# Kernel tuning notes

Measured on AMD Instinct MI355X. Metric: run time of the kernel, lower is better.

The kernel has to match this reference:

```python
import jax, jax.numpy as jnp
import numpy as np

B, T, D = 4, 2048, 2048
H = 16
DH = D // H  # 128
THETA = 10000.0


def _rope(x, offset=0):
    # x: [b, h, t, d]; lucidrains rotary_embedding_torch style (interleaved pairs)
    d = x.shape[-1]
    t = x.shape[-2]
    inv_freq = 1.0 / (THETA ** (jnp.arange(0, d, 2, dtype=jnp.float32) / d))  # [d/2]
    pos = jnp.arange(offset, offset + t, dtype=jnp.float32)
    freqs = pos[:, None] * inv_freq[None, :]              # [t, d/2]
    freqs = jnp.repeat(freqs, 2, axis=-1)                 # [t, d] (n r) interleave
    cos = jnp.cos(freqs).astype(x.dtype)
    sin = jnp.sin(freqs).astype(x.dtype)
    x1 = x[..., 0::2]
    x2 = x[..., 1::2]
    rot = jnp.stack([-x2, x1], axis=-1).reshape(x.shape)  # rotate_half
    return x * cos + rot * sin


def setup_inputs() -> dict:
    key = jax.random.key(0)
    ks = jax.random.split(key, 5)
    s = 1.0 / np.sqrt(D)
    return {
        "x": jax.random.normal(ks[0], (B, T, D), jnp.float32),
        "Wq": jax.random.normal(ks[1], (D, D), jnp.float32) * s,
        "Wk": jax.random.normal(ks[2], (D, D), jnp.float32) * s,
        "Wv": jax.random.normal(ks[3], (D, D), jnp.float32) * s,
        "Wo": jax.random.normal(ks[4], (D, D), jnp.float32) * s,
    }


def reference(x, Wq, Wk, Wv, Wo):
    b, t, d = x.shape
    # QKV projections (bias-free), split heads: b t (h f) -> b h t f
    q = (x @ Wq).reshape(b, t, H, DH).transpose(0, 2, 1, 3)
    k = (x @ Wk).reshape(b, t, H, DH).transpose(0, 2, 1, 3)
    v = (x @ Wv).reshape(b, t, H, DH).transpose(0, 2, 1, 3)
    # rotary embedding on q and k (offset = 0)
    q = _rope(q)
    k = _rope(k)
    # causal scaled dot-product attention
    scale = 1.0 / np.sqrt(DH)
    logits = jnp.einsum('bhtf,bhsf->bhts', q, k) * scale
    causal = jnp.tril(jnp.ones((t, t), dtype=bool))
    logits = jnp.where(causal, logits, jnp.finfo(logits.dtype).min)
    p = jax.nn.softmax(logits, axis=-1)
    y = jnp.einsum('bhts,bhsf->bhtf', p, v)
    # b h t f -> b t (h f), then output projection
    y = y.transpose(0, 2, 1, 3).reshape(b, t, d)
    return y @ Wo
```

## Files before the change

### kernel.cpp

```cpp
#include <hip/hip_runtime.h>
#include <hip/hip_bf16.h>
#include <math.h>

typedef unsigned short u16;
typedef __attribute__((ext_vector_type(8))) __bf16 bf16x8;
typedef __attribute__((ext_vector_type(4))) float f32x4;
typedef __attribute__((ext_vector_type(16))) float f32x16;
typedef __attribute__((ext_vector_type(8))) u16 u16x8;
typedef __attribute__((ext_vector_type(4))) u16 u16x4;
typedef __attribute__((ext_vector_type(4))) unsigned u32x4;

#define T_SEQ 2048
#define DMODEL 2048
#define NH 16
#define DHEAD 128
#define BATCH 4
#define QKV_STR 6144
#define ATTN_SCALE 0.08838834764831845f
#define QSCALE_LOG2E 0.1275411278534803f
#define ROPE_EXP_C  -0.20762050593045857f

#define GLOAD(gp, lp) __builtin_amdgcn_global_load_lds( \
    (const __attribute__((address_space(1))) void*)(gp), \
    (__attribute__((address_space(3))) void*)(lp), 16, 0, 0)

#define BAR() __builtin_amdgcn_s_barrier()
#define VMCNT4() asm volatile("s_waitcnt vmcnt(4)" ::: "memory")
#define MFMA32(A, B, C) __builtin_amdgcn_mfma_f32_32x32x16_bf16(A, B, C, 0, 0, 0)

__device__ __forceinline__ float b2f(u16 u) {
  union { float f; unsigned int i; } x; x.i = ((unsigned int)u) << 16; return x.f;
}
__device__ __forceinline__ u16 f2b(float f) {
  __bf16 h = (__bf16)f;
  return *(u16*)&h;
}
__device__ __forceinline__ unsigned pk2(float lo, float hi2) {
  __bf16 a = (__bf16)lo, b = (__bf16)hi2;
  unsigned short ua = *(unsigned short*)&a, ub = *(unsigned short*)&b;
  return (unsigned)ua | ((unsigned)ub << 16);
}

__global__ __launch_bounds__(256) void cast_f32_bf16(const float* __restrict__ in,
                                                     u16* __restrict__ out) {
  long i = ((long)blockIdx.x * 256 + threadIdx.x) * 8;
  float4 a = *(const float4*)(in + i);
  float4 b = *(const float4*)(in + i + 4);
  u16x8 r;
  r[0] = f2b(a.x); r[1] = f2b(a.y); r[2] = f2b(a.z); r[3] = f2b(a.w);
  r[4] = f2b(b.x); r[5] = f2b(b.y); r[6] = f2b(b.z); r[7] = f2b(b.w);
  *(u16x8*)(out + i) = r;
}

__global__ __launch_bounds__(256) void wtrans4_kernel(const float* __restrict__ W0,
                                                      const float* __restrict__ W1,
                                                      const float* __restrict__ W2,
                                                      const float* __restrict__ W3,
                                                      u16* __restrict__ WtBase) {
  __shared__ float tile[64][65];
  const int z = blockIdx.z;
  const float* W = (z == 0) ? W0 : (z == 1) ? W1 : (z == 2) ? W2 : W3;
  u16* Wt = WtBase + (long)z * 4194304;
  const int k0 = blockIdx.x * 64, n0 = blockIdx.y * 64;
  const int c = threadIdx.x & 63, r4 = threadIdx.x >> 6;
#pragma unroll
  for (int p = 0; p < 16; p++) {
    int r = p * 4 + r4;
    tile[r][c] = W[(long)(k0 + r) * DMODEL + n0 + c];
  }
  __syncthreads();
#pragma unroll
  for (int p = 0; p < 16; p++) {
    int r = p * 4 + r4;
    Wt[(long)(n0 + r) * DMODEL + k0 + c] = f2b(tile[c][r]);
  }
}

__global__ __launch_bounds__(256) void vtrans_kernel(const u16* __restrict__ C,
                                                     u16* __restrict__ Vt) {
  __shared__ u16 tile[64][66];
  const int s0 = blockIdx.x * 64, f0 = blockIdx.y * 64;
  const int bh = blockIdx.z;
  const int b = bh >> 4, h = bh & 15;
  const int c = threadIdx.x & 63, r4 = threadIdx.x >> 6;
#pragma unroll
  for (int p = 0; p < 16; p++) {
    int r = p * 4 + r4;
    tile[r][c] = C[(long)(b * T_SEQ + s0 + r) * QKV_STR + 4096 + h * DHEAD + f0 + c];
  }
  __syncthreads();
#pragma unroll
  for (int p = 0; p < 16; p++) {
    int r = p * 4 + r4;
    Vt[(long)(bh * DHEAD + f0 + r) * T_SEQ + s0 + c] = tile[c][r];
  }
}

__global__ __launch_bounds__(256) void rope_k_kernel(u16* __restrict__ X) {
  int idx = blockIdx.x * 256 + threadIdx.x;
  int c8 = idx & 255;
  long row = idx >> 8;
  int t = (int)(row & (T_SEQ - 1));
  int i4 = c8 & 15;
  long off = row * QKV_STR + 2048 + (long)c8 * 8;
  u16x8 v = *(u16x8*)(X + off);
  float o[8];
#pragma unroll
  for (int j = 0; j < 4; j++) {
    int i = i4 * 4 + j;
    float inv = __builtin_amdgcn_exp2f((float)i * ROPE_EXP_C);
    float ang = (float)t * inv;
    float cs = __cosf(ang), sn = __sinf(ang);
    float x0 = b2f(v[2 * j]), x1 = b2f(v[2 * j + 1]);
    o[2 * j]     = x0 * cs - x1 * sn;
    o[2 * j + 1] = x1 * cs + x0 * sn;
  }
  u16x8 r;
#pragma unroll
  for (int j = 0; j < 8; j++) r[j] = f2b(o[j]);
  *(u16x8*)(X + off) = r;
}

#define LOAD_A(q)                                                      \
  _Pragma("unroll") for (int k = 0; k < 2; k++)                        \
  _Pragma("unroll") for (int m = 0; m < 2; m++) {                      \
    int r = wr * 128 + (q) * 32 + m * 16 + lr;                         \
    int cc = (k * 4 + lc) ^ (r & 7);                                   \
    a[k][m] = *(const bf16x8*)&sA[par][r * 64 + cc * 8];               \
  }

#define LOAD_B()                                                       \
  _Pragma("unroll") for (int k = 0; k < 2; k++)                        \
  _Pragma("unroll") for (int n = 0; n < 4; n++) {                      \
    int r = wc * 64 + n * 16 + lr;                                     \
    int cc = (k * 4 + lc) ^ (r & 7);                                   \
    b[k][n] = *(const bf16x8*)&sB[par][r * 64 + cc * 8];               \
  }

#define MFMA_QUAD(q)                                                   \
  _Pragma("unroll") for (int k = 0; k < 2; k++)                        \
  _Pragma("unroll") for (int n = 0; n < 4; n++)                        \
  _Pragma("unroll") for (int m = 0; m < 2; m++)                        \
    acc[(q) * 2 + m][n] = __builtin_amdgcn_mfma_f32_16x16x32_bf16(     \
        a[k][m], b[k][n], acc[(q) * 2 + m][n], 0, 0, 0);

#define STAGE_HALF(g, ld, ldsp, rc0, t_, h_)                           \
  _Pragma("unroll") for (int j = 0; j < 2; j++) {                      \
    int rl = (h_) * 128 + wid * 16 + j * 8 + (lane >> 3);              \
    int cc = (lane & 7) ^ (lane >> 3);                                 \
    GLOAD((g) + ((rc0) + rl) * (long)(ld) + (long)(t_) * 64 + cc * 8,  \
          (ldsp) + (h_) * 128 * 64 + (wid * 16 + j * 8) * 64);         \
  }

template <int OUT_F32>
__global__ __launch_bounds__(512, 2) void gemm_bt(const u16* __restrict__ A, long lda,
                                                  const u16* __restrict__ Bt,
                                                  void* __restrict__ Cv,
                                                  int M, int N, int K) {
  __shared__ u16 sA[2][256 * 64];
  __shared__ u16 sB[2][256 * 64];
  const int tid = threadIdx.x, lane = tid & 63, wid = tid >> 6;
  const int wr = wid >> 2, wc = wid & 3;
  const int lr = lane & 15, lc = lane >> 4;
  const int id = blockIdx.x;
  const int per = (N >> 8) >> 3;
  const int g8 = id >> 3;
  const long col0 = (long)((id & 7) + 8 * (g8 % per)) * 256;
  const long row0 = (long)(g8 / per) * 256;
  const int NT = K >> 6;

  f32x4 acc[8][4] = {};
  bf16x8 a[2][2], b[2][4];

  STAGE_HALF(Bt, K, &sB[0][0], col0, 0, 0);
  STAGE_HALF(Bt, K, &sB[0][0], col0, 0, 1);
  STAGE_HALF(A, lda, &sA[0][0], row0, 0, 0);
  STAGE_HALF(A, lda, &sA[0][0], row0, 0, 1);
  STAGE_HALF(Bt, K, &sB[1][0], col0, 1, 0);
  STAGE_HALF(Bt, K, &sB[1][0], col0, 1, 1);
  VMCNT4();
  BAR();

#pragma unroll 2
  for (int t = 0; t < NT; t++) {
    const int par = t & 1;
    LOAD_B();
    LOAD_A(0);
    if (t + 1 < NT) { STAGE_HALF(A, lda, &sA[par ^ 1][0], row0, t + 1, 0); }
    BAR();
    __builtin_amdgcn_s_setprio(1); MFMA_QUAD(0); __builtin_amdgcn_s_setprio(0);
    BAR();
    LOAD_A(1);
    if (t + 1 < NT) { STAGE_HALF(A, lda, &sA[par ^ 1][0], row0, t + 1, 1); }
    if (t + 2 < NT) { STAGE_HALF(Bt, K, &sB[par][0], col0, t + 2, 0); }
    BAR();
    __builtin_amdgcn_s_setprio(1); MFMA_QUAD(1); __builtin_amdgcn_s_setprio(0);
    BAR();
    LOAD_A(2);
    if (t + 2 < NT) { STAGE_HALF(Bt, K, &sB[par][0], col0, t + 2, 1); }
    BAR();
    __builtin_amdgcn_s_setprio(1); MFMA_QUAD(2); __builtin_amdgcn_s_setprio(0);
    BAR();
    LOAD_A(3);
    VMCNT4();
    BAR();
    __builtin_amdgcn_s_setprio(1); MFMA_QUAD(3); __builtin_amdgcn_s_setprio(0);
    BAR();
  }

#pragma unroll
  for (int mf = 0; mf < 8; mf++)
#pragma unroll
    for (int n = 0; n < 4; n++)
#pragma unroll
      for (int i = 0; i < 4; i++) {
        long row = row0 + wr * 128 + mf * 16 + lc * 4 + i;
        long col = col0 + wc * 64 + n * 16 + lr;
        float v = acc[mf][n][i];
        if (OUT_F32) ((float*)Cv)[row * N + col] = v;
        else ((u16*)Cv)[row * N + col] = f2b(v);
      }
}

__global__ __launch_bounds__(256, 2) void attn_kernel(const u16* __restrict__ QK,
                                                      const u16* __restrict__ Vt) {
  __shared__ u16 lK[2][64 * 128];
  __shared__ u16 lV[2][128 * 64];
  const int tid = threadIdx.x, lane = tid & 63, w = tid >> 6;
  const int hi = lane >> 5, l31 = lane & 31;
  const int id = blockIdx.x;
  const int qt = 15 - (id >> 6);
  const int bh = id & 63;
  const int b = bh >> 4, h = bh & 15;
  const int qg = qt * 128 + w * 32 + l31;
  const int swz = l31 & 7;

  bf16x8 qf[8];
  const long qrow = (long)(b * T_SEQ + qg) * QKV_STR + h * DHEAD;
#pragma unroll
  for (int kd = 0; kd < 8; kd++) {
    u16x8 raw = *(const u16x8*)(QK + qrow + kd * 16 + hi * 8);
    bf16x8 q;
#pragma unroll
    for (int jj = 0; jj < 4; jj++) {
      int pi = kd * 8 + hi * 4 + jj;
      float ang = (float)qg * __builtin_amdgcn_exp2f((float)pi * ROPE_EXP_C);
      float cs = __cosf(ang), sn = __sinf(ang);
      float x0 = b2f(raw[2 * jj]), x1 = b2f(raw[2 * jj + 1]);
      q[2 * jj]     = (__bf16)((x0 * cs - x1 * sn) * QSCALE_LOG2E);
      q[2 * jj + 1] = (__bf16)((x1 * cs + x0 * sn) * QSCALE_LOG2E);
    }
    qf[kd] = q;
  }

  f32x16 o0 = {}, o1 = {}, o2 = {}, o3 = {};
  float m_st = -INFINITY, l_st = 0.f;
  const int nt = (qt + 1) * 2;

#define STAGE(nb, kt_)                                                              \
  {                                                                                 \
    _Pragma("unroll")                                                               \
    for (int j = 0; j < 4; j++) {                                                   \
      int sb = (w * 4 + j) * 64;                                                    \
      int slot = sb + lane;                                                         \
      { int r = slot >> 4, pc = slot & 15, cc = pc ^ (r & 7);                       \
        GLOAD(QK + (long)(b * T_SEQ + (kt_) * 64 + r) * QKV_STR + 2048 +            \
                  h * DHEAD + cc * 8,                                               \
              &lK[nb][sb * 8]); }                                                   \
      { int r = slot >> 3, pc = slot & 7, cc = pc ^ (r & 7);                        \
        GLOAD(Vt + (long)(bh * DHEAD + r) * T_SEQ + (kt_) * 64 + cc * 8,            \
              &lV[nb][sb * 8]); }                                                   \
    }                                                                               \
  }

  STAGE(0, 0);
  __syncthreads();

  for (int kt = 0; kt < nt; kt++) {
    const int cur = kt & 1;
    if (kt + 1 < nt) STAGE(cur ^ 1, kt + 1);

    f32x16 st0 = {}, st1 = {};
    __builtin_amdgcn_s_setprio(1);
#pragma unroll
    for (int kd = 0; kd < 8; kd++) {
      int pc = (kd * 2 + hi) ^ swz;
      bf16x8 kf0 = *(const bf16x8*)&lK[cur][l31 * 128 + pc * 8];
      bf16x8 kf1 = *(const bf16x8*)&lK[cur][(32 + l31) * 128 + pc * 8];
      st0 = MFMA32(kf0, qf[kd], st0);
      st1 = MFMA32(kf1, qf[kd], st1);
    }
    __builtin_amdgcn_s_setprio(0);

    if (kt * 64 + 63 > qt * 128 + w * 32) {
#pragma unroll
      for (int r = 0; r < 16; r++) {
        int sl = kt * 64 + (r & 3) + 8 * (r >> 2) + 4 * hi;
        if (sl > qg) st0[r] = -1e30f;
        if (sl + 32 > qg) st1[r] = -1e30f;
      }
    }

    float mx = -1e30f;
#pragma unroll
    for (int r = 0; r < 16; r++) mx = fmaxf(mx, fmaxf(st0[r], st1[r]));
    mx = fmaxf(mx, __shfl_xor(mx, 32, 64));
    if (__any(mx > m_st + 8.0f)) {
      float mnew = fmaxf(m_st, mx);
      float corr = __builtin_amdgcn_exp2f(m_st - mnew);
      m_st = mnew;
      l_st *= corr;
#pragma unroll
      for (int r = 0; r < 16; r++) {
        o0[r] *= corr; o1[r] *= corr; o2[r] *= corr; o3[r] *= corr;
      }
    }
    float rs = 0.f;
#pragma unroll
    for (int r = 0; r < 16; r++) {
      st0[r] = __builtin_amdgcn_exp2f(st0[r] - m_st); rs += st0[r];
      st1[r] = __builtin_amdgcn_exp2f(st1[r] - m_st); rs += st1[r];
    }
    l_st += rs + __shfl_xor(rs, 32, 64);

    __builtin_amdgcn_s_setprio(1);
#define PVHALF(stX, sb)                                                        \
    _Pragma("unroll")                                                          \
    for (int g = 0; g < 2; g++) {                                              \
      unsigned A0 = pk2(stX[8 * g + 0], stX[8 * g + 1]);                       \
      unsigned A1 = pk2(stX[8 * g + 2], stX[8 * g + 3]);                       \
      unsigned B0 = pk2(stX[8 * g + 4], stX[8 * g + 5]);                       \
      unsigned B1 = pk2(stX[8 * g + 6], stX[8 * g + 7]);                       \
      unsigned r0 = __shfl_xor(hi ? A0 : B0, 32, 64);                          \
      unsigned r1 = __shfl_xor(hi ? A1 : B1, 32, 64);                          \
      u32x4 pw;                                                                \
      pw[0] = hi ? r0 : A0;                                                    \
      pw[1] = hi ? r1 : A1;                                                    \
      pw[2] = hi ? B0 : r0;                                                    \
      pw[3] = hi ? B1 : r1;                                                    \
      bf16x8 pa = *(bf16x8*)&pw;                                               \
      const int ks = (sb) * 2 + g;                                             \
      int pc0 = (ks * 2 + hi) ^ swz;                                           \
      bf16x8 vb0 = *(const bf16x8*)&lV[cur][(l31) * 64 + pc0 * 8];             \
      o0 = MFMA32(vb0, pa, o0);                                                \
      bf16x8 vb1 = *(const bf16x8*)&lV[cur][(32 + l31) * 64 + pc0 * 8];        \
      o1 = MFMA32(vb1, pa, o1);                                                \
      bf16x8 vb2 = *(const bf16x8*)&lV[cur][(64 + l31) * 64 + pc0 * 8];        \
      o2 = MFMA32(vb2, pa, o2);                                                \
      bf16x8 vb3 = *(const bf16x8*)&lV[cur][(96 + l31) * 64 + pc0 * 8];        \
      o3 = MFMA32(vb3, pa, o3);                                                \
    }
    PVHALF(st0, 0)
    PVHALF(st1, 1)
#undef PVHALF
    __builtin_amdgcn_s_setprio(0);

    __syncthreads();
  }

  float inv = __builtin_amdgcn_rcpf(l_st);
#define WR(oN, n)                                                              \
  _Pragma("unroll")                                                            \
  for (int rq = 0; rq < 4; rq++) {                                             \
    u16x4 pk;                                                                  \
    _Pragma("unroll")                                                          \
    for (int j = 0; j < 4; j++) pk[j] = f2b(oN[rq * 4 + j] * inv);             \
    *(u16x4*)((u16*)QK + qrow + 4096 + (n) * 32 + rq * 8 + hi * 4) = pk;       \
  }
  WR(o0, 0) WR(o1, 1) WR(o2, 2) WR(o3, 3)
#undef WR
#undef STAGE
}

extern "C" void kernel_launch(void* const* d_in, const int* in_sizes, int n_in,
                              void* d_out, int out_size, void* d_ws, size_t ws_size,
                              hipStream_t stream) {
  const float* x  = (const float*)d_in[0];
  const float* Wq = (const float*)d_in[1];
  const float* Wk = (const float*)d_in[2];
  const float* Wv = (const float*)d_in[3];
  const float* Wo = (const float*)d_in[4];
  float* out = (float*)d_out;
  char* ws = (char*)d_ws;

  const long MB = 1048576L;
  u16* xb   = (u16*)(ws);
  u16* Wt4  = (u16*)(ws + 32 * MB);
  u16* Cqkv = (u16*)(ws + 64 * MB);
  u16* Vtb  = xb;

  cast_f32_bf16<<<8192, 256, 0, stream>>>(x, xb);
  dim3 wt_g(32, 32, 4);
  wtrans4_kernel<<<wt_g, 256, 0, stream>>>(Wq, Wk, Wv, Wo, Wt4);

  gemm_bt<0><<<768, 512, 0, stream>>>(xb, 2048, Wt4, Cqkv, 8192, 6144, 2048);

  rope_k_kernel<<<8192, 256, 0, stream>>>(Cqkv);

  dim3 vt_g(32, 2, 64);
  vtrans_kernel<<<vt_g, 256, 0, stream>>>(Cqkv, Vtb);

  attn_kernel<<<1024, 256, 0, stream>>>(Cqkv, Vtb);

  gemm_bt<1><<<256, 512, 0, stream>>>(Cqkv + 4096, QKV_STR, Wt4 + 3 * 4194304L,
                                      (void*)out, 8192, 2048, 2048);
}
```

Measured before the change: 432.0 us.

## Single-buffer V tile with split vmcnt waits to fit three attention blocks per CU

The attention kernel keeps K double-buffered but drops V to a single LDS buffer. This cuts shared memory per block from 64KB to 48KB so launch bounds can request 3 blocks per CU. V for the next tile is now issued after the PV MFMAs finish. Explicit vmcnt waits and barriers let the QK^T stage start once K has landed while V is still in flight. In exchange, V loads overlap only with the next QK^T and softmax, and the tighter register budget of 3 blocks per CU may cause spills.

```diff
diff --git a/kernel.cpp b/kernel.cpp
--- a/kernel.cpp
+++ b/kernel.cpp
@@ -222,10 +222,10 @@
       }
 }
 
-__global__ __launch_bounds__(256, 2) void attn_kernel(const u16* __restrict__ QK,
+__global__ __launch_bounds__(256, 3) void attn_kernel(const u16* __restrict__ QK,
                                                       const u16* __restrict__ Vt) {
   __shared__ u16 lK[2][64 * 128];
-  __shared__ u16 lV[2][128 * 64];
+  __shared__ u16 lV[128 * 64];
   const int tid = threadIdx.x, lane = tid & 63, w = tid >> 6;
   const int hi = lane >> 5, l31 = lane & 31;
   const int id = blockIdx.x;
@@ -257,28 +257,41 @@
   float m_st = -INFINITY, l_st = 0.f;
   const int nt = (qt + 1) * 2;
 
-#define STAGE(nb, kt_)                                                              \
+#define STAGE_K(nb, kt_)                                                            \
   {                                                                                 \
     _Pragma("unroll")                                                               \
     for (int j = 0; j < 4; j++) {                                                   \
       int sb = (w * 4 + j) * 64;                                                    \
       int slot = sb + lane;                                                         \
-      { int r = slot >> 4, pc = slot & 15, cc = pc ^ (r & 7);                       \
-        GLOAD(QK + (long)(b * T_SEQ + (kt_) * 64 + r) * QKV_STR + 2048 +            \
-                  h * DHEAD + cc * 8,                                               \
-              &lK[nb][sb * 8]); }                                                   \
-      { int r = slot >> 3, pc = slot & 7, cc = pc ^ (r & 7);                        \
-        GLOAD(Vt + (long)(bh * DHEAD + r) * T_SEQ + (kt_) * 64 + cc * 8,            \
-              &lV[nb][sb * 8]); }                                                   \
+      int r = slot >> 4, pc = slot & 15, cc = pc ^ (r & 7);                         \
+      GLOAD(QK + (long)(b * T_SEQ + (kt_) * 64 + r) * QKV_STR + 2048 +              \
+                h * DHEAD + cc * 8,                                                 \
+            &lK[nb][sb * 8]);                                                       \
     }                                                                               \
   }
-
-  STAGE(0, 0);
-  __syncthreads();
+#define STAGE_V(kt_)                                                                \
+  {                                                                                 \
+    _Pragma("unroll")                                                               \
+    for (int j = 0; j < 4; j++) {                                                   \
+      int sb = (w * 4 + j) * 64;                                                    \
+      int slot = sb + lane;                                                         \
+      int r = slot >> 3, pc = slot & 7, cc = pc ^ (r & 7);                          \
+      GLOAD(Vt + (long)(bh * DHEAD + r) * T_SEQ + (kt_) * 64 + cc * 8,              \
+            &lV[sb * 8]);                                                           \
+    }                                                                               \
+  }
+
+  STAGE_K(0, 0);
+  STAGE_V(0);
 
   for (int kt = 0; kt < nt; kt++) {
     const int cur = kt & 1;
-    if (kt + 1 < nt) STAGE(cur ^ 1, kt + 1);
+    const bool more = (kt + 1 < nt);
+    if (more) STAGE_K(cur ^ 1, kt + 1);
+
+    if (more) { asm volatile("s_waitcnt vmcnt(8)" ::: "memory"); }
+    else      { asm volatile("s_waitcnt vmcnt(4)" ::: "memory"); }
+    BAR();
 
     f32x16 st0 = {}, st1 = {};
     __builtin_amdgcn_s_setprio(1);
@@ -322,6 +335,10 @@
       st1[r] = __builtin_amdgcn_exp2f(st1[r] - m_st); rs += st1[r];
     }
     l_st += rs + __shfl_xor(rs, 32, 64);
+
+    if (more) { asm volatile("s_waitcnt vmcnt(4)" ::: "memory"); }
+    else      { asm volatile("s_waitcnt vmcnt(0)" ::: "memory"); }
+    BAR();
 
     __builtin_amdgcn_s_setprio(1);
 #define PVHALF(stX, sb)                                                        \
@@ -341,13 +358,13 @@
       bf16x8 pa = *(bf16x8*)&pw;                                               \
       const int ks = (sb) * 2 + g;                                             \
       int pc0 = (ks * 2 + hi) ^ swz;                                           \
-      bf16x8 vb0 = *(const bf16x8*)&lV[cur][(l31) * 64 + pc0 * 8];             \
+      bf16x8 vb0 = *(const bf16x8*)&lV[(l31) * 64 + pc0 * 8];                  \
       o0 = MFMA32(vb0, pa, o0);                                                \
-      bf16x8 vb1 = *(const bf16x8*)&lV[cur][(32 + l31) * 64 + pc0 * 8];        \
+      bf16x8 vb1 = *(const bf16x8*)&lV[(32 + l31) * 64 + pc0 * 8];             \
       o1 = MFMA32(vb1, pa, o1);                                                \
-      bf16x8 vb2 = *(const bf16x8*)&lV[cur][(64 + l31) * 64 + pc0 * 8];        \
+      bf16x8 vb2 = *(const bf16x8*)&lV[(64 + l31) * 64 + pc0 * 8];             \
       o2 = MFMA32(vb2, pa, o2);                                                \
-      bf16x8 vb3 = *(const bf16x8*)&lV[cur][(96 + l31) * 64 + pc0 * 8];        \
+      bf16x8 vb3 = *(const bf16x8*)&lV[(96 + l31) * 64 + pc0 * 8];             \
       o3 = MFMA32(vb3, pa, o3);                                                \
     }
     PVHALF(st0, 0)
@@ -355,7 +372,8 @@
 #undef PVHALF
     __builtin_amdgcn_s_setprio(0);
 
-    __syncthreads();
+    BAR();
+    if (more) STAGE_V(kt + 1);
   }
 
   float inv = __builtin_amdgcn_rcpf(l_st);
@@ -369,7 +387,8 @@
   }
   WR(o0, 0) WR(o1, 1) WR(o2, 2) WR(o3, 3)
 #undef WR
-#undef STAGE
+#undef STAGE_K
+#undef STAGE_V
 }
 
 extern "C" void kernel_launch(void* const* d_in, const int* in_sizes, int n_in,
```

Measured after the change: 494.2 us. 1.14x slower.

## Fuse V transpose into QKV GEMM epilogue and drop vtrans kernel

Applied to the files above, without the earlier changes.

The QKV GEMM epilogue now writes V tiles already transposed into a separate Vt buffer, staging them through LDS with a swizzled layout. This removes the standalone vtrans kernel and its extra global read/write of V. Q and K are stored with a narrower 4096 stride, and attention writes Y to its own buffer. The cost is a more complex epilogue with an LDS round-trip in the V blocks.

```diff
diff --git a/kernel.cpp b/kernel.cpp
--- a/kernel.cpp
+++ b/kernel.cpp
@@ -15,7 +15,7 @@
 #define NH 16
 #define DHEAD 128
 #define BATCH 4
-#define QKV_STR 6144
+#define QK_STR 4096
 #define ATTN_SCALE 0.08838834764831845f
 #define QSCALE_LOG2E 0.1275411278534803f
 #define ROPE_EXP_C  -0.20762050593045857f
@@ -76,33 +76,13 @@
   }
 }
 
-__global__ __launch_bounds__(256) void vtrans_kernel(const u16* __restrict__ C,
-                                                     u16* __restrict__ Vt) {
-  __shared__ u16 tile[64][66];
-  const int s0 = blockIdx.x * 64, f0 = blockIdx.y * 64;
-  const int bh = blockIdx.z;
-  const int b = bh >> 4, h = bh & 15;
-  const int c = threadIdx.x & 63, r4 = threadIdx.x >> 6;
-#pragma unroll
-  for (int p = 0; p < 16; p++) {
-    int r = p * 4 + r4;
-    tile[r][c] = C[(long)(b * T_SEQ + s0 + r) * QKV_STR + 4096 + h * DHEAD + f0 + c];
-  }
-  __syncthreads();
-#pragma unroll
-  for (int p = 0; p < 16; p++) {
-    int r = p * 4 + r4;
-    Vt[(long)(bh * DHEAD + f0 + r) * T_SEQ + s0 + c] = tile[c][r];
-  }
-}
-
 __global__ __launch_bounds__(256) void rope_k_kernel(u16* __restrict__ X) {
   int idx = blockIdx.x * 256 + threadIdx.x;
   int c8 = idx & 255;
   long row = idx >> 8;
   int t = (int)(row & (T_SEQ - 1));
   int i4 = c8 & 15;
-  long off = row * QKV_STR + 2048 + (long)c8 * 8;
+  long off = row * QK_STR + 2048 + (long)c8 * 8;
   u16x8 v = *(u16x8*)(X + off);
   float o[8];
 #pragma unroll
@@ -126,7 +106,7 @@
   _Pragma("unroll") for (int m = 0; m < 2; m++) {                      \
     int r = wr * 128 + (q) * 32 + m * 16 + lr;                         \
     int cc = (k * 4 + lc) ^ (r & 7);                                   \
-    a[k][m] = *(const bf16x8*)&sA[par][r * 64 + cc * 8];               \
+    a[k][m] = *(const bf16x8*)&sAb[par * 16384 + r * 64 + cc * 8];     \
   }
 
 #define LOAD_B()                                                       \
@@ -134,7 +114,7 @@
   _Pragma("unroll") for (int n = 0; n < 4; n++) {                      \
     int r = wc * 64 + n * 16 + lr;                                     \
     int cc = (k * 4 + lc) ^ (r & 7);                                   \
-    b[k][n] = *(const bf16x8*)&sB[par][r * 64 + cc * 8];               \
+    b[k][n] = *(const bf16x8*)&sBb[par * 16384 + r * 64 + cc * 8];     \
   }
 
 #define MFMA_QUAD(q)                                                   \
@@ -152,13 +132,15 @@
           (ldsp) + (h_) * 128 * 64 + (wid * 16 + j * 8) * 64);         \
   }
 
-template <int OUT_F32>
+template <int OUT_F32, int VWRITE>
 __global__ __launch_bounds__(512, 2) void gemm_bt(const u16* __restrict__ A, long lda,
                                                   const u16* __restrict__ Bt,
-                                                  void* __restrict__ Cv,
+                                                  void* __restrict__ Cv, long ldc,
+                                                  u16* __restrict__ VtOut,
                                                   int M, int N, int K) {
-  __shared__ u16 sA[2][256 * 64];
-  __shared__ u16 sB[2][256 * 64];
+  __shared__ u16 smem[65536];
+  u16* sAb = smem;
+  u16* sBb = smem + 32768;
   const int tid = threadIdx.x, lane = tid & 63, wid = tid >> 6;
   const int wr = wid >> 2, wc = wid & 3;
   const int lr = lane & 15, lc = lane >> 4;
@@ -172,12 +154,12 @@
   f32x4 acc[8][4] = {};
   bf16x8 a[2][2], b[2][4];
 
-  STAGE_HALF(Bt, K, &sB[0][0], col0, 0, 0);
-  STAGE_HALF(Bt, K, &sB[0][0], col0, 0, 1);
-  STAGE_HALF(A, lda, &sA[0][0], row0, 0, 0);
-  STAGE_HALF(A, lda, &sA[0][0], row0, 0, 1);
-  STAGE_HALF(Bt, K, &sB[1][0], col0, 1, 0);
-  STAGE_HALF(Bt, K, &sB[1][0], col0, 1, 1);
+  STAGE_HALF(Bt, K, sBb, col0, 0, 0);
+  STAGE_HALF(Bt, K, sBb, col0, 0, 1);
+  STAGE_HALF(A, lda, sAb, row0, 0, 0);
+  STAGE_HALF(A, lda, sAb, row0, 0, 1);
+  STAGE_HALF(Bt, K, sBb + 16384, col0, 1, 0);
+  STAGE_HALF(Bt, K, sBb + 16384, col0, 1, 1);
   VMCNT4();
   BAR();
 
@@ -186,18 +168,18 @@
     const int par = t & 1;
     LOAD_B();
     LOAD_A(0);
-    if (t + 1 < NT) { STAGE_HALF(A, lda, &sA[par ^ 1][0], row0, t + 1, 0); }
+    if (t + 1 < NT) { STAGE_HALF(A, lda, sAb + (par ^ 1) * 16384, row0, t + 1, 0); }
     BAR();
     __builtin_amdgcn_s_setprio(1); MFMA_QUAD(0); __builtin_amdgcn_s_setprio(0);
     BAR();
     LOAD_A(1);
-    if (t + 1 < NT) { STAGE_HALF(A, lda, &sA[par ^ 1][0], row0, t + 1, 1); }
-    if (t + 2 < NT) { STAGE_HALF(Bt, K, &sB[par][0], col0, t + 2, 0); }
+    if (t + 1 < NT) { STAGE_HALF(A, lda, sAb + (par ^ 1) * 16384, row0, t + 1, 1); }
+    if (t + 2 < NT) { STAGE_HALF(Bt, K, sBb + par * 16384, col0, t + 2, 0); }
     BAR();
     __builtin_amdgcn_s_setprio(1); MFMA_QUAD(1); __builtin_amdgcn_s_setprio(0);
     BAR();
     LOAD_A(2);
-    if (t + 2 < NT) { STAGE_HALF(Bt, K, &sB[par][0], col0, t + 2, 1); }
+    if (t + 2 < NT) { STAGE_HALF(Bt, K, sBb + par * 16384, col0, t + 2, 1); }
     BAR();
     __builtin_amdgcn_s_setprio(1); MFMA_QUAD(2); __builtin_amdgcn_s_setprio(0);
     BAR();
@@ -208,22 +190,51 @@
     BAR();
   }
 
-#pragma unroll
-  for (int mf = 0; mf < 8; mf++)
-#pragma unroll
-    for (int n = 0; n < 4; n++)
-#pragma unroll
-      for (int i = 0; i < 4; i++) {
-        long row = row0 + wr * 128 + mf * 16 + lc * 4 + i;
-        long col = col0 + wc * 64 + n * 16 + lr;
-        float v = acc[mf][n][i];
-        if (OUT_F32) ((float*)Cv)[row * N + col] = v;
-        else ((u16*)Cv)[row * N + col] = f2b(v);
-      }
+  if (VWRITE && col0 >= 4096) {
+    u16* scr = smem + wid * 8192;
+#pragma unroll
+    for (int mf = 0; mf < 8; mf++)
+#pragma unroll
+      for (int n = 0; n < 4; n++)
+#pragma unroll
+        for (int i = 0; i < 4; i++) {
+          int sl = mf * 16 + lc * 4 + i;
+          int fr = n * 16 + lr;
+          scr[fr * 128 + (((sl >> 3) ^ (fr & 7)) << 3) + (sl & 7)] = f2b(acc[mf][n][i]);
+        }
+    asm volatile("s_waitcnt lgkmcnt(0)" ::: "memory");
+    const int h0 = (int)((col0 - 4096) >> 7) + (wc >> 1);
+    const int f00 = (wc & 1) * 64;
+    const long rowbase = row0 + wr * 128;
+    const int bb = (int)(rowbase >> 11);
+    const int s0 = (int)(rowbase & 2047);
+#pragma unroll
+    for (int c = 0; c < 16; c++) {
+      int fr = c * 4 + (lane >> 4);
+      int pc = (lane & 15) ^ (fr & 7);
+      u16x8 vv = *(u16x8*)&scr[fr * 128 + pc * 8];
+      *(u16x8*)(VtOut + ((long)((bb * 16 + h0) * 128 + f00 + fr)) * 2048 +
+                s0 + (lane & 15) * 8) = vv;
+    }
+  } else {
+#pragma unroll
+    for (int mf = 0; mf < 8; mf++)
+#pragma unroll
+      for (int n = 0; n < 4; n++)
+#pragma unroll
+        for (int i = 0; i < 4; i++) {
+          long row = row0 + wr * 128 + mf * 16 + lc * 4 + i;
+          long col = col0 + wc * 64 + n * 16 + lr;
+          float v = acc[mf][n][i];
+          if (OUT_F32) ((float*)Cv)[row * ldc + col] = v;
+          else ((u16*)Cv)[row * ldc + col] = f2b(v);
+        }
+  }
 }
 
 __global__ __launch_bounds__(256, 2) void attn_kernel(const u16* __restrict__ QK,
-                                                      const u16* __restrict__ Vt) {
+                                                      const u16* __restrict__ Vt,
+                                                      u16* __restrict__ Y) {
   __shared__ u16 lK[2][64 * 128];
   __shared__ u16 lV[2][128 * 64];
   const int tid = threadIdx.x, lane = tid & 63, w = tid >> 6;
@@ -236,7 +247,7 @@
   const int swz = l31 & 7;
 
   bf16x8 qf[8];
-  const long qrow = (long)(b * T_SEQ + qg) * QKV_STR + h * DHEAD;
+  const long qrow = (long)(b * T_SEQ + qg) * QK_STR + h * DHEAD;
 #pragma unroll
   for (int kd = 0; kd < 8; kd++) {
     u16x8 raw = *(const u16x8*)(QK + qrow + kd * 16 + hi * 8);
@@ -264,7 +275,7 @@
       int sb = (w * 4 + j) * 64;                                                    \
       int slot = sb + lane;                                                         \
       { int r = slot >> 4, pc = slot & 15, cc = pc ^ (r & 7);                       \
-        GLOAD(QK + (long)(b * T_SEQ + (kt_) * 64 + r) * QKV_STR + 2048 +            \
+        GLOAD(QK + (long)(b * T_SEQ + (kt_) * 64 + r) * QK_STR + 2048 +             \
                   h * DHEAD + cc * 8,                                               \
               &lK[nb][sb * 8]); }                                                   \
       { int r = slot >> 3, pc = slot & 7, cc = pc ^ (r & 7);                        \
@@ -359,13 +370,14 @@
   }
 
   float inv = __builtin_amdgcn_rcpf(l_st);
+  const long yrow = (long)(b * T_SEQ + qg) * 2048 + h * DHEAD;
 #define WR(oN, n)                                                              \
   _Pragma("unroll")                                                            \
   for (int rq = 0; rq < 4; rq++) {                                             \
     u16x4 pk;                                                                  \
     _Pragma("unroll")                                                          \
     for (int j = 0; j < 4; j++) pk[j] = f2b(oN[rq * 4 + j] * inv);             \
-    *(u16x4*)((u16*)QK + qrow + 4096 + (n) * 32 + rq * 8 + hi * 4) = pk;       \
+    *(u16x4*)(Y + yrow + (n) * 32 + rq * 8 + hi * 4) = pk;                     \
   }
   WR(o0, 0) WR(o1, 1) WR(o2, 2) WR(o3, 3)
 #undef WR
@@ -384,24 +396,24 @@
   char* ws = (char*)d_ws;
 
   const long MB = 1048576L;
-  u16* xb   = (u16*)(ws);
-  u16* Wt4  = (u16*)(ws + 32 * MB);
-  u16* Cqkv = (u16*)(ws + 64 * MB);
-  u16* Vtb  = xb;
+  u16* xb  = (u16*)(ws);
+  u16* Wt4 = (u16*)(ws + 32 * MB);
+  u16* Cqk = (u16*)(ws + 64 * MB);
+  u16* Vtb = (u16*)(ws + 128 * MB);
+  u16* Yb  = xb;
 
   cast_f32_bf16<<<8192, 256, 0, stream>>>(x, xb);
   dim3 wt_g(32, 32, 4);
   wtrans4_kernel<<<wt_g, 256, 0, stream>>>(Wq, Wk, Wv, Wo, Wt4);
 
-  gemm_bt<0><<<768, 512, 0, stream>>>(xb, 2048, Wt4, Cqkv, 8192, 6144, 2048);
-
-  rope_k_kernel<<<8192, 256, 0, stream>>>(Cqkv);
-
-  dim3 vt_g(32, 2, 64);
-  vtrans_kernel<<<vt_g, 256, 0, stream>>>(Cqkv, Vtb);
-
-  attn_kernel<<<1024, 256, 0, stream>>>(Cqkv, Vtb);
-
-  gemm_bt<1><<<256, 512, 0, stream>>>(Cqkv + 4096, QKV_STR, Wt4 + 3 * 4194304L,
-                                      (void*)out, 8192, 2048, 2048);
-}
+  gemm_bt<0, 1><<<768, 512, 0, stream>>>(xb, 2048, Wt4, Cqk, 4096, Vtb,
+                                         8192, 6144, 2048);
+
+  rope_k_kernel<<<8192, 256, 0, stream>>>(Cqk);
+
+  attn_kernel<<<1024, 256, 0, stream>>>(Cqk, Vtb, Yb);
+
+  gemm_bt<1, 0><<<256, 512, 0, stream>>>(Yb, 2048, Wt4 + 3 * 4194304L,
+                                         (void*)out, 2048, nullptr,
+                                         8192, 2048, 2048);
+}
```

Result: faster. 408.4 us, median of 2 (-5.5%).
